# Performance work log

Hardware: AMD Instinct MI355X
Metric: run time of the kernel (lower is better)

## Reference

```python
import jax, jax.numpy as jnp
import numpy as np
from jax import lax

NUM_ENT = 100000
NUM_REL = 100          # init_rel has 2*NUM_REL rows (forward + inverse relations)
DIM = 200              # init_dim = gcn_dim = embed_dim
E = 1000000
B = 1024
K_H, K_W = 10, 20      # embed_dim == k_h * k_w
NUM_FILT = 200
KER = 7
FLAT_H = 2 * K_H - KER + 1   # 14
FLAT_W = K_W - KER + 1       # 14
FLAT_SZ = FLAT_H * FLAT_W * NUM_FILT  # 39200


def _bn1d(x, g, b, eps=1e-5):
    # training-mode BatchNorm1d (biased variance, matching torch)
    m = x.mean(0)
    v = x.var(0)
    return (x - m) * lax.rsqrt(v + eps) * g + b


def _bn2d(x, g, b, eps=1e-5):
    m = x.mean((0, 2, 3), keepdims=True)
    v = x.var((0, 2, 3), keepdims=True)
    return (x - m) * lax.rsqrt(v + eps) * g[None, :, None, None] + b[None, :, None, None]


def _compgcn_layer(x, r, src, dst, etype, enorm,
                   w_in, w_out, w_loop, w_rel, loop_rel, bias, gamma, beta):
    # CompGCNCov with opn='mult': comp(h_src, rel) = h_src * rel
    half = etype.shape[0] // 2
    comp = x[src] * r[etype]                                   # [E, din] edge gather + compose
    msg = jnp.concatenate([comp[:half] @ w_in,                 # first half: original edges
                           comp[half:] @ w_out], axis=0)       # second half: inverse edges
    msg = msg * enorm[:, None]
    agg = jax.ops.segment_sum(msg, dst, num_segments=NUM_ENT)  # scatter-sum to dst nodes
    loop = (x * loop_rel) @ w_loop                             # self-loop composition
    h = (agg + loop) * (1.0 / 3.0) + bias
    h = _bn1d(h, gamma, beta)
    return jnp.tanh(h), r @ w_rel


def setup_inputs() -> dict:
    key = jax.random.key(0)
    ks = jax.random.split(key, 40)
    f32 = jnp.float32
    s = 1.0 / np.sqrt(DIM)
    inp = {
        "init_embed": jax.random.normal(ks[0], (NUM_ENT, DIM), f32) * s,
        "init_rel":   jax.random.normal(ks[1], (2 * NUM_REL, DIM), f32) * s,
        "edge_norm":  jax.random.uniform(ks[2], (E,), f32),
    }
    names = ["w_in", "w_out", "w_loop", "w_rel"]
    for layer in (1, 2):
        for i, n in enumerate(names):
            inp[f"{n}{layer}"] = jax.random.normal(ks[3 + 6 * layer + i], (DIM, DIM), f32) * s
        inp[f"loop_rel{layer}"] = jax.random.normal(jax.random.fold_in(key, layer), (1, DIM), f32) * s
        inp[f"b{layer}"] = jnp.zeros((DIM,), f32)
        inp[f"g{layer}"] = jnp.ones((DIM,), f32)
        inp[f"be{layer}"] = jnp.zeros((DIM,), f32)
    inp["conv_w"] = jax.random.normal(ks[20], (NUM_FILT, 1, KER, KER), f32) * (1.0 / KER)
    inp["conv_b"] = jnp.zeros((NUM_FILT,), f32)
    inp["fc_w"] = jax.random.normal(ks[21], (DIM, FLAT_SZ), f32) * (1.0 / np.sqrt(FLAT_SZ))
    inp["fc_b"] = jnp.zeros((DIM,), f32)
    for n, c in (("bn0", 1), ("bn1", NUM_FILT), ("bn2", DIM)):
        inp[f"{n}_g"] = jnp.ones((c,), f32)
        inp[f"{n}_b"] = jnp.zeros((c,), f32)
    inp["subj"] = jax.random.randint(ks[22], (B,), 0, NUM_ENT)
    inp["rel_idx"] = jax.random.randint(ks[23], (B,), 0, 2 * NUM_REL)
    inp["obj"] = jax.random.randint(ks[24], (B,), 0, NUM_ENT)
    inp["src"] = jax.random.randint(ks[25], (E,), 0, NUM_ENT)
    inp["dst"] = jax.random.randint(ks[26], (E,), 0, NUM_ENT)
    inp["edge_type"] = jnp.concatenate([
        jax.random.randint(ks[27], (E // 2,), 0, NUM_REL),          # in-edges
        jax.random.randint(ks[28], (E // 2,), NUM_REL, 2 * NUM_REL)])  # inverse edges
    return inp


def reference(init_embed, init_rel, edge_norm,
              w_in1, w_out1, w_loop1, w_rel1, loop_rel1, b1, g1, be1,
              w_in2, w_out2, w_loop2, w_rel2, loop_rel2, b2, g2, be2,
              conv_w, conv_b, fc_w, fc_b,
              bn0_g, bn0_b, bn1_g, bn1_b, bn2_g, bn2_b,
              subj, rel_idx, obj, src, dst, edge_type):
    # --- GCN encoder: 2 CompGCN layers ---
    x, r = _compgcn_layer(init_embed, init_rel, src, dst, edge_type, edge_norm,
                          w_in1, w_out1, w_loop1, w_rel1, loop_rel1, b1, g1, be1)
    x, r = _compgcn_layer(x, r, src, dst, edge_type, edge_norm,
                          w_in2, w_out2, w_loop2, w_rel2, loop_rel2, b2, g2, be2)
    sub_emb, rel_emb, obj_emb = x[subj], r[rel_idx], x[obj]   # [B, DIM] each
    # --- ConvE scoring head ---
    stk = jnp.concatenate([sub_emb[:, None, :], rel_emb[:, None, :]], 1)
    stk = stk.reshape(B, 1, 2 * K_H, K_W)                     # [B,1,20,20]
    h = _bn2d(stk, bn0_g, bn0_b)
    h = lax.conv_general_dilated(h, conv_w, (1, 1), 'VALID',
                                 dimension_numbers=('NCHW', 'OIHW', 'NCHW'))
    h = h + conv_b[None, :, None, None]                       # [B,NUM_FILT,14,14]
    h = jnp.maximum(_bn2d(h, bn1_g, bn1_b), 0.0)
    h = h.reshape(B, FLAT_SZ) @ fc_w.T + fc_b                 # [B, DIM]
    h = jnp.maximum(_bn1d(h, bn2_g, bn2_b), 0.0)
    return jax.nn.sigmoid(h @ obj_emb.T)                      # [B, B]
```

## Files before the change

### kernel.cpp

```cpp
#include <hip/hip_runtime.h>

#define DIM 200
#define NENT 100000
#define NEDGE 1000000
#define EHALF 500000
#define NB 1024
#define NFILT 200
#define FLATSZ 39200

#define NDF ((size_t)NENT * DIM)
#define REGF ((size_t)20100000)

#define PANEL_TOT_H 6656
#define Y1OFF_H 3584
#define WT_TOTAL_H 139776

typedef float floatx4 __attribute__((ext_vector_type(4)));
typedef _Float16 halfx8 __attribute__((ext_vector_type(8)));
typedef _Float16 halfx4 __attribute__((ext_vector_type(4)));

__device__ __forceinline__ void gAtomicAdd(float* p, float v) { unsafeAtomicAdd(p, v); }
__device__ __forceinline__ void gAtomicAdd(double* p, double v) { unsafeAtomicAdd(p, v); }

__device__ __forceinline__ void gload16h(const _Float16* g, _Float16* l) {
    __builtin_amdgcn_global_load_lds(
        (const __attribute__((address_space(1))) void*)g,
        (__attribute__((address_space(3))) void*)l,
        16, 0, 0);
}

__global__ __launch_bounds__(256) void edge_hist(
    const int* __restrict__ dst, int* __restrict__ hist)
{
    int stride = gridDim.x * blockDim.x;
    for (int e = blockIdx.x * 256 + threadIdx.x; e < NEDGE; e += stride)
        atomicAdd(&hist[dst[e]], 1);
}

__global__ __launch_bounds__(256) void scan1(
    const int* __restrict__ hist, int* __restrict__ incl, int* __restrict__ bsum)
{
    __shared__ int sm[256];
    int i = blockIdx.x * 256 + threadIdx.x;
    int t = threadIdx.x;
    sm[t] = (i < NENT) ? hist[i] : 0;
    __syncthreads();
    for (int off = 1; off < 256; off <<= 1) {
        int v = (t >= off) ? sm[t - off] : 0;
        __syncthreads();
        sm[t] += v;
        __syncthreads();
    }
    if (i < NENT) incl[i] = sm[t];
    if (t == 255) bsum[blockIdx.x] = sm[255];
}

__global__ __launch_bounds__(512) void scan2(int* bsum, int nb)
{
    __shared__ int sm[512];
    int t = threadIdx.x;
    int v = (t < nb) ? bsum[t] : 0;
    sm[t] = v;
    __syncthreads();
    for (int off = 1; off < 512; off <<= 1) {
        int u = (t >= off) ? sm[t - off] : 0;
        __syncthreads();
        sm[t] += u;
        __syncthreads();
    }
    if (t < nb) bsum[t] = sm[t] - v;
}

__global__ __launch_bounds__(256) void scan3(
    const int* __restrict__ hist, int* __restrict__ offs,
    const int* __restrict__ bsum, int* __restrict__ cursor)
{
    int i = blockIdx.x * 256 + threadIdx.x;
    if (i < NENT) {
        int excl = offs[i] - hist[i] + bsum[blockIdx.x];
        offs[i] = excl;
        cursor[i] = excl;
    }
    if (i == 0) offs[NENT] = NEDGE;
}

__global__ __launch_bounds__(256) void edge_fill(
    const int* __restrict__ src, const int* __restrict__ dst,
    const int* __restrict__ etype, const float* __restrict__ enorm,
    int* __restrict__ cursor, int4* __restrict__ recs)
{
    int stride = gridDim.x * blockDim.x;
    for (int e = blockIdx.x * 256 + threadIdx.x; e < NEDGE; e += stride) {
        int pos = atomicAdd(&cursor[dst[e]], 1);
        recs[pos] = make_int4(src[e], etype[e] | ((e >= EHALF) ? 0x10000 : 0),
                              __float_as_int(enorm[e]), 0);
    }
}

__global__ __launch_bounds__(256) void build_map(
    const int* __restrict__ subj, const int* __restrict__ obj, int* __restrict__ map)
{
    int i = blockIdx.x * 256 + threadIdx.x;
    if (i < NB) map[subj[i]] = i;
    else if (i < 2 * NB) map[obj[i - NB]] = i;
}

__global__ __launch_bounds__(256) void to_f16(
    const float* __restrict__ X, _Float16* __restrict__ Y, long n4)
{
    long stride = (long)gridDim.x * blockDim.x;
    for (long i = (long)blockIdx.x * blockDim.x + threadIdx.x; i < n4; i += stride) {
        float4 v = ((const float4*)X)[i];
        halfx4 h;
        h[0] = (_Float16)v.x; h[1] = (_Float16)v.y;
        h[2] = (_Float16)v.z; h[3] = (_Float16)v.w;
        ((halfx4*)Y)[i] = h;
    }
}

__global__ __launch_bounds__(256) void gather_nodes(
    const _Float16* __restrict__ x16, const float* __restrict__ r,
    const int* __restrict__ offs, const int4* __restrict__ recs,
    _Float16* __restrict__ aggI, _Float16* __restrict__ aggO)
{
    int node = blockIdx.x * 4 + (threadIdx.x >> 6);
    int lane = threadIdx.x & 63;
    if (node >= NENT) return;
    int beg = offs[node], end = offs[node + 1];
    bool act = lane < 50;
    int lane_c = min(lane, 49);
    const float4* rb = (const float4*)r;
    float4 aI = make_float4(0.f, 0.f, 0.f, 0.f);
    float4 aO = make_float4(0.f, 0.f, 0.f, 0.f);

    auto ld_x = [&](int s) -> float4 {
        halfx4 v = *(const halfx4*)&x16[(size_t)s * 200 + lane_c * 4];
        return make_float4((float)v[0], (float)v[1], (float)v[2], (float)v[3]);
    };

    if (beg < end) {
        int i1 = min(beg + 1, end - 1);
        int4 rcA = recs[beg];
        int4 rcB = recs[i1];
        float4 xvA = ld_x(rcA.x);
        float4 rvA = rb[(size_t)(rcA.y & 0xffff) * 50 + lane_c];
        for (int i = beg; i < end; ++i) {
            int i2 = min(i + 2, end - 1);
            int4 rcC = recs[i2];
            float4 xvB = ld_x(rcB.x);
            float4 rvB = rb[(size_t)(rcB.y & 0xffff) * 50 + lane_c];
            float w = __int_as_float(rcA.z);
            float wI = (rcA.y & 0x10000) ? 0.f : w;
            float wO = w - wI;
            float px = xvA.x * rvA.x, py = xvA.y * rvA.y,
                  pz = xvA.z * rvA.z, pw = xvA.w * rvA.w;
            aI.x += px * wI; aI.y += py * wI; aI.z += pz * wI; aI.w += pw * wI;
            aO.x += px * wO; aO.y += py * wO; aO.z += pz * wO; aO.w += pw * wO;
            rcA = rcB; rcB = rcC; xvA = xvB; rvA = rvB;
        }
    }
    if (act) {
        halfx4 hI, hO;
        hI[0] = (_Float16)aI.x; hI[1] = (_Float16)aI.y;
        hI[2] = (_Float16)aI.z; hI[3] = (_Float16)aI.w;
        hO[0] = (_Float16)aO.x; hO[1] = (_Float16)aO.y;
        hO[2] = (_Float16)aO.z; hO[3] = (_Float16)aO.w;
        size_t base = (size_t)node * 200 + lane * 4;
        *(halfx4*)&aggI[base] = hI;
        *(halfx4*)&aggO[base] = hO;
    }
}

__global__ __launch_bounds__(256) void pack_w3(
    const float* __restrict__ w0, const float* __restrict__ w1,
    const float* __restrict__ w2, const float* __restrict__ lrel,
    _Float16* __restrict__ WpP)
{
    int i = blockIdx.x * 256 + threadIdx.x;
    if (i >= WT_TOTAL_H) return;
    int p = i / PANEL_TOT_H;
    int r = i % PANEL_TOT_H;
    int y = (r >= Y1OFF_H) ? 1 : 0;
    int rr = y ? (r - Y1OFF_H) : r;
    int rl = rr >> 5;
    int qx = (rr >> 3) & 3;
    int e = rr & 7;
    int q = qx ^ ((rl >> 1) & 3);
    int n = y * 112 + rl;
    int seg = p / 7, c = p - seg * 7;
    int k = c * 32 + q * 8 + e;
    const float* W = (seg == 0) ? w0 : (seg == 1) ? w1 : w2;
    float v = (n < 200 && k < 200) ? W[k * 200 + n] : 0.f;
    if (seg == 2 && n < 200 && k < 200) v *= lrel[k];
    WpP[i] = (_Float16)v;
}

__global__ __launch_bounds__(256) void pack_fcw(
    const float* __restrict__ W, _Float16* __restrict__ Wt)
{
    long i = (long)blockIdx.x * 256 + threadIdx.x;
    if (i >= (long)208 * FLATSZ) return;
    int n = (int)(i / FLATSZ);
    Wt[i] = (n < 200) ? (_Float16)W[i] : (_Float16)0.f;
}

template<int Y>
__global__ __launch_bounds__(1024) void gemm_big(
    const _Float16* __restrict__ A0h, const _Float16* __restrict__ A1h,
    const _Float16* __restrict__ A2h, const _Float16* __restrict__ WpP,
    float* __restrict__ C, const float* __restrict__ bias,
    const int* __restrict__ map, float alpha,
    double* __restrict__ s1, double* __restrict__ s2)
{
    constexpr int NF = Y ? 6 : 7;
    constexpr int PC = NF;
    constexpr int PANEL_H = NF * 512;
    constexpr int YOFF_H = Y ? Y1OFF_H : 0;
    constexpr int SEG_LDS_H = 7 * PANEL_H;
    __shared__ _Float16 Sb[2 * SEG_LDS_H];
    __shared__ float fsum[NF * 16];
    __shared__ float fsq[NF * 16];

    int tid = threadIdx.x;
    int lane = tid & 63, wave = tid >> 6;
    int col16 = lane & 15, quad = lane >> 4;
    if (tid < NF * 16) { fsum[tid] = 0.f; fsq[tid] = 0.f; }

    int gw = blockIdx.x * 16 + wave;
    bool act = gw < 3125;
    int t = act ? gw : 0;
    int r0 = t * 32 + col16, r1 = r0 + 16;
    size_t b0 = (size_t)r0 * 200, b1 = (size_t)r1 * 200;

    floatx4 acc[NF][2];
#pragma unroll
    for (int nf = 0; nf < NF; ++nf) { acc[nf][0] = (floatx4)0.f; acc[nf][1] = (floatx4)0.f; }

    halfx8 ca0, ca1, na0, na1;

    auto stage = [&](int seg, int bufi) {
        for (int cc = wave; cc < 7 * PC; cc += 16) {
            int p7 = cc / PC, sub = cc - p7 * PC;
            const _Float16* g = WpP + (size_t)(seg * 7 + p7) * PANEL_TOT_H
                              + YOFF_H + sub * 512 + lane * 8;
            gload16h(g, Sb + bufi * SEG_LDS_H + cc * 512);
        }
    };
    auto loadA = [&](int kc, halfx8& a0, halfx8& a1) {
        int seg = kc / 7, c = kc - seg * 7;
        int koff = c * 32 + quad * 8;
        if (koff < 200) {
            const _Float16* A = (seg == 0) ? A0h : (seg == 1) ? A1h : A2h;
            a0 = *(const halfx8*)&A[b0 + koff];
            a1 = *(const halfx8*)&A[b1 + koff];
        } else {
            a0 = (halfx8)0; a1 = (halfx8)0;
        }
    };

    stage(0, 0);
    if (act) loadA(0, ca0, ca1);
    __syncthreads();

    int buf = 0;
    for (int seg = 0; seg < 3; ++seg) {
        if (seg < 2) stage(seg + 1, buf ^ 1);
        if (act) {
#pragma unroll
            for (int c = 0; c < 7; ++c) {
                int kc = seg * 7 + c;
                if (kc < 20) loadA(kc + 1, na0, na1);
                const _Float16* P = Sb + buf * SEG_LDS_H + c * PANEL_H;
                __builtin_amdgcn_s_setprio(1);
#pragma unroll
                for (int nf = 0; nf < NF; ++nf) {
                    int rl = nf * 16 + col16;
                    int qs = quad ^ ((rl >> 1) & 3);
                    halfx8 b = *(const halfx8*)&P[rl * 32 + qs * 8];
                    acc[nf][0] = __builtin_amdgcn_mfma_f32_16x16x32_f16(ca0, b, acc[nf][0], 0, 0, 0);
                    acc[nf][1] = __builtin_amdgcn_mfma_f32_16x16x32_f16(ca1, b, acc[nf][1], 0, 0, 0);
                }
                __builtin_amdgcn_s_setprio(0);
                ca0 = na0; ca1 = na1;
            }
        }
        __syncthreads();
        buf ^= 1;
    }

    int slot[2][4];
    if (map && act) {
#pragma unroll
        for (int h = 0; h < 2; ++h)
#pragma unroll
            for (int j = 0; j < 4; ++j)
                slot[h][j] = map[t * 32 + h * 16 + quad * 4 + j];
    }
    if (act) {
#pragma unroll
        for (int nf = 0; nf < NF; ++nf) {
            int lc = nf * 16 + col16;
            int colg = Y * 112 + lc;
            float ls = 0.f, lq = 0.f;
            if (colg < 200) {
                float bv = bias[colg];
#pragma unroll
                for (int h = 0; h < 2; ++h) {
                    int rbase = t * 32 + h * 16 + quad * 4;
#pragma unroll
                    for (int j = 0; j < 4; ++j) {
                        float v = acc[nf][h][j] * alpha + bv;
                        ls += v; lq += v * v;
                        if (!map) {
                            C[(size_t)(rbase + j) * 200 + colg] = v;
                        } else {
                            int s = slot[h][j];
                            if (s >= 0) C[(size_t)s * 200 + colg] = v;
                        }
                    }
                }
            }
            ls += __shfl_down(ls, 32); ls += __shfl_down(ls, 16);
            lq += __shfl_down(lq, 32); lq += __shfl_down(lq, 16);
            if (quad == 0 && colg < 200) {
                atomicAdd(&fsum[lc], ls);
                atomicAdd(&fsq[lc], lq);
            }
        }
    }
    __syncthreads();
    if (tid < NF * 16) {
        int colg = Y * 112 + tid;
        if (colg < 200) {
            gAtomicAdd(&s1[colg], (double)fsum[tid]);
            gAtomicAdd(&s2[colg], (double)fsq[tid]);
        }
    }
}

template<int NF0, int NF>
__device__ __forceinline__ void fc_gemm_body(
    const _Float16* __restrict__ Ph, const _Float16* __restrict__ Wt,
    float* __restrict__ part, int ky, _Float16* Bs)
{
    int t = threadIdx.x;
    int lane = t & 63, wave = t >> 6;
    int col16 = lane & 15, quad = lane >> 4;
    int row_base = blockIdx.x * 128 + wave * 32;
    int c0 = ky * 25;
    floatx4 acc[NF][2];
#pragma unroll
    for (int nf = 0; nf < NF; ++nf) { acc[nf][0] = (floatx4)0.f; acc[nf][1] = (floatx4)0.f; }
    int r0 = row_base + col16, r1 = row_base + 16 + col16;
    const int rows4 = NF * 16 * 4;

    for (int c = c0; c < c0 + 25; ++c) {
        int k0 = c * 32;
        for (int i = t; i < rows4; i += 256) {
            int nl = i >> 2, part_i = i & 3;
            int n = NF0 * 16 + nl;
            *(halfx8*)&Bs[nl * 40 + part_i * 8] =
                *(const halfx8*)&Wt[(size_t)n * FLATSZ + k0 + part_i * 8];
        }
        __syncthreads();
        int koff = k0 + quad * 8;
        halfx8 a0 = *(const halfx8*)&Ph[(size_t)r0 * FLATSZ + koff];
        halfx8 a1 = *(const halfx8*)&Ph[(size_t)r1 * FLATSZ + koff];
#pragma unroll
        for (int nf = 0; nf < NF; ++nf) {
            halfx8 b = *(const halfx8*)&Bs[(nf * 16 + col16) * 40 + quad * 8];
            acc[nf][0] = __builtin_amdgcn_mfma_f32_16x16x32_f16(a0, b, acc[nf][0], 0, 0, 0);
            acc[nf][1] = __builtin_amdgcn_mfma_f32_16x16x32_f16(a1, b, acc[nf][1], 0, 0, 0);
        }
        __syncthreads();
    }
    float* out = part + (size_t)ky * (NB * 200);
#pragma unroll
    for (int nf = 0; nf < NF; ++nf) {
        int colg = NF0 * 16 + nf * 16 + col16;
        if (colg >= 200) continue;
#pragma unroll
        for (int h = 0; h < 2; ++h) {
            int rbase = row_base + h * 16 + quad * 4;
#pragma unroll
            for (int j = 0; j < 4; ++j)
                out[(size_t)(rbase + j) * 200 + colg] = acc[nf][h][j];
        }
    }
}

__global__ __launch_bounds__(256) void fc_gemm(
    const _Float16* __restrict__ Ph, const _Float16* __restrict__ Wt,
    float* __restrict__ part)
{
    __shared__ _Float16 Bs[112 * 40];
    int ky = blockIdx.y >> 1;
    if ((blockIdx.y & 1) == 0)
        fc_gemm_body<0, 7>(Ph, Wt, part, ky, Bs);
    else
        fc_gemm_body<7, 6>(Ph, Wt, part, ky, Bs);
}

__global__ __launch_bounds__(256) void fc_reduce(
    const float* __restrict__ part, const float* __restrict__ bias,
    float* __restrict__ hfc)
{
    int i = blockIdx.x * 256 + threadIdx.x;
    float acc = bias[i % 200];
#pragma unroll
    for (int y = 0; y < 49; ++y) acc += part[(size_t)y * (NB * 200) + i];
    hfc[i] = acc;
}

__global__ __launch_bounds__(256) void colstats(
    const float* __restrict__ X, int M, int rpb,
    double* __restrict__ s1, double* __restrict__ s2)
{
    int c = threadIdx.x;
    if (c >= 200) return;
    int r0 = blockIdx.x * rpb;
    int r1 = min(r0 + rpb, M);
    float sum = 0.f, sq = 0.f;
    for (int rr = r0; rr < r1; ++rr) {
        float v = X[(size_t)rr * 200 + c];
        sum += v; sq += v * v;
    }
    gAtomicAdd(&s1[c], (double)sum);
    gAtomicAdd(&s2[c], (double)sq);
}

__global__ void finalize_stats(const double* __restrict__ s1, const double* __restrict__ s2,
                               const float* __restrict__ g, const float* __restrict__ bb,
                               float* __restrict__ sc, float* __restrict__ sh,
                               int ncols, double count)
{
    int c = threadIdx.x;
    if (c >= ncols) return;
    double m = s1[c] / count;
    double v = s2[c] / count - m * m;
    double scd = (double)g[c] / sqrt(v + 1e-5);
    sc[c] = (float)scd;
    sh[c] = (float)((double)bb[c] - m * scd);
}

__global__ __launch_bounds__(256) void bn_tanh_f16(
    const float* __restrict__ X, const float* __restrict__ sc,
    const float* __restrict__ sh, _Float16* __restrict__ Y, long n4)
{
    long stride = (long)gridDim.x * blockDim.x;
    for (long i = (long)blockIdx.x * blockDim.x + threadIdx.x; i < n4; i += stride) {
        int c4 = (int)(i % 50) * 4;
        float4 v = ((const float4*)X)[i];
        halfx4 h;
        h[0] = (_Float16)tanhf(v.x * sc[c4 + 0] + sh[c4 + 0]);
        h[1] = (_Float16)tanhf(v.y * sc[c4 + 1] + sh[c4 + 1]);
        h[2] = (_Float16)tanhf(v.z * sc[c4 + 2] + sh[c4 + 2]);
        h[3] = (_Float16)tanhf(v.w * sc[c4 + 3] + sh[c4 + 3]);
        ((halfx4*)Y)[i] = h;
    }
}

__global__ __launch_bounds__(256) void bn_act_200(
    float* __restrict__ X, const float* __restrict__ sc, const float* __restrict__ sh,
    long n4, int act)
{
    long stride = (long)gridDim.x * blockDim.x;
    for (long i = (long)blockIdx.x * blockDim.x + threadIdx.x; i < n4; i += stride) {
        int c4 = (int)(i % 50) * 4;
        float4 v = ((const float4*)X)[i];
        float a0 = v.x * sc[c4 + 0] + sh[c4 + 0];
        float a1 = v.y * sc[c4 + 1] + sh[c4 + 1];
        float a2 = v.z * sc[c4 + 2] + sh[c4 + 2];
        float a3 = v.w * sc[c4 + 3] + sh[c4 + 3];
        if (act == 0) { a0 = tanhf(a0); a1 = tanhf(a1); a2 = tanhf(a2); a3 = tanhf(a3); }
        else { a0 = fmaxf(a0, 0.f); a1 = fmaxf(a1, 0.f); a2 = fmaxf(a2, 0.f); a3 = fmaxf(a3, 0.f); }
        ((float4*)X)[i] = make_float4(a0, a1, a2, a3);
    }
}

__global__ __launch_bounds__(256) void rel_mm(
    const float* __restrict__ R, const float* __restrict__ W, float* __restrict__ O)
{
    int idx = blockIdx.x * blockDim.x + threadIdx.x;
    if (idx >= 200 * 200) return;
    int row = idx / 200, col = idx - row * 200;
    float acc = 0.f;
    for (int k = 0; k < 200; ++k) acc = fmaf(R[row * 200 + k], W[k * 200 + col], acc);
    O[idx] = acc;
}

__global__ __launch_bounds__(256) void build_stk(
    const float* __restrict__ x2c, const float* __restrict__ r2,
    const int* __restrict__ subj, const int* __restrict__ ridx,
    const int* __restrict__ map,
    float* __restrict__ stk, double* __restrict__ s1, double* __restrict__ s2)
{
    __shared__ float wsum[4], wsq[4];
    int b = blockIdx.x, t = threadIdx.x;
    const float* se = x2c + (size_t)map[subj[b]] * DIM;
    const float* re = r2 + (size_t)ridx[b] * DIM;
    float sum = 0.f, sq = 0.f;
    for (int i = t; i < 400; i += 256) {
        float v = (i < 200) ? se[i] : re[i - 200];
        stk[(size_t)b * 400 + i] = v;
        sum += v; sq += v * v;
    }
    for (int off = 32; off > 0; off >>= 1) {
        sum += __shfl_down(sum, off);
        sq  += __shfl_down(sq, off);
    }
    if ((t & 63) == 0) { wsum[t >> 6] = sum; wsq[t >> 6] = sq; }
    __syncthreads();
    if (t == 0) {
        float S = wsum[0] + wsum[1] + wsum[2] + wsum[3];
        float Q = wsq[0] + wsq[1] + wsq[2] + wsq[3];
        gAtomicAdd(&s1[0], (double)S);
        gAtomicAdd(&s2[0], (double)Q);
    }
}

__global__ __launch_bounds__(256) void conv_fwd(
    const float* __restrict__ stk, const float* __restrict__ conv_w,
    const float* __restrict__ conv_b, const float* __restrict__ sc0,
    const float* __restrict__ sh0, _Float16* __restrict__ Ph,
    double* __restrict__ s1, double* __restrict__ s2)
{
    __shared__ float img[400];
    __shared__ float wsm[9800];
    __shared__ float bsm[200];
    __shared__ float fsum[200];
    __shared__ float fsq[200];
    int b = blockIdx.x, t = threadIdx.x;
    float scale0 = sc0[0], shift0 = sh0[0];
    if (t < 200) { fsum[t] = 0.f; fsq[t] = 0.f; bsm[t] = conv_b[t]; }
    for (int i = t; i < 400; i += 256) img[i] = stk[(size_t)b * 400 + i] * scale0 + shift0;
    for (int i = t; i < 9800; i += 256) wsm[i] = conv_w[i];
    __syncthreads();
    for (int fy = t; fy < 2800; fy += 256) {
        int f = fy / 14, y = fy - (fy / 14) * 14;
        const float* wf = &wsm[f * 49];
        float acc[14];
        float bias = bsm[f];
#pragma unroll
        for (int xx = 0; xx < 14; ++xx) acc[xx] = bias;
#pragma unroll
        for (int i = 0; i < 7; ++i) {
            const float* rowp = &img[(y + i) * 20];
            float rv[20];
#pragma unroll
            for (int c = 0; c < 20; ++c) rv[c] = rowp[c];
#pragma unroll
            for (int j = 0; j < 7; ++j) {
                float wv = wf[i * 7 + j];
#pragma unroll
                for (int xx = 0; xx < 14; ++xx) acc[xx] = fmaf(rv[xx + j], wv, acc[xx]);
            }
        }
        float ls = 0.f, lq = 0.f;
        _Float16* pp = Ph + (size_t)b * FLATSZ + (size_t)f * 196 + y * 14;
#pragma unroll
        for (int xx = 0; xx < 14; ++xx) {
            float v = acc[xx];
            pp[xx] = (_Float16)v;
            ls += v; lq += v * v;
        }
        atomicAdd(&fsum[f], ls);
        atomicAdd(&fsq[f], lq);
    }
    __syncthreads();
    if (t < 200) {
        gAtomicAdd(&s1[t], (double)fsum[t]);
        gAtomicAdd(&s2[t], (double)fsq[t]);
    }
}

__global__ __launch_bounds__(256) void bn1_relu_f16(
    _Float16* __restrict__ Ph, const float* __restrict__ sc, const float* __restrict__ sh)
{
    long n4 = (long)NB * (FLATSZ / 4);
    long stride = (long)gridDim.x * blockDim.x;
    for (long i = (long)blockIdx.x * blockDim.x + threadIdx.x; i < n4; i += stride) {
        int k4 = (int)(i % (FLATSZ / 4));
        int f = k4 / 49;
        float s = sc[f], h = sh[f];
        halfx4 v = ((const halfx4*)Ph)[i];
#pragma unroll
        for (int e = 0; e < 4; ++e) {
            float x = (float)v[e];
            x = fmaxf(x * s + h, 0.f);
            v[e] = (_Float16)x;
        }
        ((halfx4*)Ph)[i] = v;
    }
}

__global__ __launch_bounds__(256) void score_mm(
    const float* __restrict__ Hn, const float* __restrict__ x2c,
    const int* __restrict__ obj, const int* __restrict__ map,
    float* __restrict__ out)
{
    __shared__ float Asm[16][17];
    __shared__ float Bsm[16][17];
    int tx = threadIdx.x & 15, ty = threadIdx.x >> 4;
    int row = blockIdx.y * 16 + ty;
    int col = blockIdx.x * 16 + tx;
    int oj = map[obj[blockIdx.x * 16 + ty]];
    float acc = 0.f;
    for (int k0 = 0; k0 < 200; k0 += 16) {
        int k = k0 + tx;
        Asm[ty][tx] = (k < 200) ? Hn[(size_t)row * 200 + k] : 0.f;
        Bsm[ty][tx] = (k < 200) ? x2c[(size_t)oj * 200 + k] : 0.f;
        __syncthreads();
#pragma unroll
        for (int kk = 0; kk < 16; ++kk) acc = fmaf(Asm[ty][kk], Bsm[tx][kk], acc);
        __syncthreads();
    }
    out[(size_t)row * NB + col] = 1.f / (1.f + expf(-acc));
}

extern "C" void kernel_launch(void* const* d_in, const int* in_sizes, int n_in,
                              void* d_out, int out_size, void* d_ws, size_t ws_size,
                              hipStream_t stream)
{
    (void)in_sizes; (void)n_in; (void)out_size;
    const float* init_embed = (const float*)d_in[0];
    const float* init_rel   = (const float*)d_in[1];
    const float* edge_norm  = (const float*)d_in[2];
    const float* w_in1  = (const float*)d_in[3];
    const float* w_out1 = (const float*)d_in[4];
    const float* w_loop1= (const float*)d_in[5];
    const float* w_rel1 = (const float*)d_in[6];
    const float* lrel1  = (const float*)d_in[7];
    const float* b1     = (const float*)d_in[8];
    const float* gm1    = (const float*)d_in[9];
    const float* be1    = (const float*)d_in[10];
    const float* w_in2  = (const float*)d_in[11];
    const float* w_out2 = (const float*)d_in[12];
    const float* w_loop2= (const float*)d_in[13];
    const float* w_rel2 = (const float*)d_in[14];
    const float* lrel2  = (const float*)d_in[15];
    const float* b2     = (const float*)d_in[16];
    const float* gm2    = (const float*)d_in[17];
    const float* be2    = (const float*)d_in[18];
    const float* conv_w = (const float*)d_in[19];
    const float* conv_b = (const float*)d_in[20];
    const float* fc_w   = (const float*)d_in[21];
    const float* fc_b   = (const float*)d_in[22];
    const float* bn0_g  = (const float*)d_in[23];
    const float* bn0_b  = (const float*)d_in[24];
    const float* bn1_g  = (const float*)d_in[25];
    const float* bn1_b  = (const float*)d_in[26];
    const float* bn2_g  = (const float*)d_in[27];
    const float* bn2_b  = (const float*)d_in[28];
    const int* subj   = (const int*)d_in[29];
    const int* relidx = (const int*)d_in[30];
    const int* obj    = (const int*)d_in[31];
    const int* src    = (const int*)d_in[32];
    const int* dst    = (const int*)d_in[33];
    const int* etype  = (const int*)d_in[34];

    float* ws = (float*)d_ws;
    float* R0 = ws;
    float* R1 = ws + REGF;
    float* R2 = ws + 2 * REGF;
    float* p = ws + 3 * REGF;
    float* r1v = p;            p += 40000;
    float* r2v = p;            p += 40000;
    float* stk = p;            p += 409600;
    float* hfc = p;            p += 204800;
    float* x2c = p;            p += 409600;
    float* fsc = p;            p += 256;
    float* fsh = p;            p += 256;
    double* ds1 = (double*)p;  p += 512;
    double* ds2 = (double*)p;  p += 512;
    _Float16* Wp = (_Float16*)p; p += (WT_TOTAL_H + 1) / 2;
    int* map = (int*)p;        p += NENT;
    int* hist = (int*)p;       p += NENT;
    int* offs = (int*)p;       p += NENT + 4;
    int* cursor = (int*)p;     p += NENT;
    int* bsum = (int*)p;       p += 512;
    int4* recs = (int4*)p;     p += (size_t)NEDGE * 4;

    float* x1f = R0;
    _Float16* aggI1 = (_Float16*)R1;
    _Float16* ie16  = (_Float16*)(R1 + 10050000);
    _Float16* aggOh = (_Float16*)R2;
    _Float16* x1h = (_Float16*)R1;
    _Float16* aggI2 = (_Float16*)R0;
    _Float16* Ph  = (_Float16*)R0;
    _Float16* fch = (_Float16*)R2;
    float* fpart = R2 + 4200000;

    const size_t NEED = (size_t)(p - ws) * sizeof(float);
    if (ws_size < NEED) return;

    const int NBLK = (NENT + 255) / 256;
    const size_t DSBYTES = 512 * sizeof(double);

    hipMemsetAsync(hist, 0, NENT * sizeof(int), stream);
    hipMemsetAsync(map, 0xFF, NENT * sizeof(int), stream);
    edge_hist<<<1024, 256, 0, stream>>>(dst, hist);
    scan1<<<NBLK, 256, 0, stream>>>(hist, offs, bsum);
    scan2<<<1, 512, 0, stream>>>(bsum, NBLK);
    scan3<<<NBLK, 256, 0, stream>>>(hist, offs, bsum, cursor);
    edge_fill<<<1024, 256, 0, stream>>>(src, dst, etype, edge_norm, cursor, recs);
    build_map<<<(2 * NB + 255) / 256, 256, 0, stream>>>(subj, obj, map);

    const int PACK_BLKS = (WT_TOTAL_H + 255) / 256;

    pack_w3<<<PACK_BLKS, 256, 0, stream>>>(w_in1, w_out1, w_loop1, lrel1, Wp);
    to_f16<<<4096, 256, 0, stream>>>(init_embed, ie16, (long)NENT * 50);
    gather_nodes<<<(NENT + 3) / 4, 256, 0, stream>>>(ie16, init_rel, offs, recs,
                                                     aggI1, aggOh);
    hipMemsetAsync(ds1, 0, DSBYTES, stream);
    gemm_big<0><<<256, 1024, 0, stream>>>(aggI1, aggOh, ie16, Wp,
                                          x1f, b1, nullptr, 1.f / 3.f, ds1, ds2);
    gemm_big<1><<<256, 1024, 0, stream>>>(aggI1, aggOh, ie16, Wp,
                                          x1f, b1, nullptr, 1.f / 3.f, ds1, ds2);
    finalize_stats<<<1, 256, 0, stream>>>(ds1, ds2, gm1, be1, fsc, fsh, 200, (double)NENT);
    bn_tanh_f16<<<4096, 256, 0, stream>>>(x1f, fsc, fsh, x1h, (long)NENT * 50);
    rel_mm<<<(40000 + 255) / 256, 256, 0, stream>>>(init_rel, w_rel1, r1v);

    pack_w3<<<PACK_BLKS, 256, 0, stream>>>(w_in2, w_out2, w_loop2, lrel2, Wp);
    gather_nodes<<<(NENT + 3) / 4, 256, 0, stream>>>(x1h, r1v, offs, recs,
                                                     aggI2, aggOh);
    hipMemsetAsync(ds1, 0, DSBYTES, stream);
    gemm_big<0><<<256, 1024, 0, stream>>>(aggI2, aggOh, x1h, Wp,
                                          x2c, b2, map, 1.f / 3.f, ds1, ds2);
    gemm_big<1><<<256, 1024, 0, stream>>>(aggI2, aggOh, x1h, Wp,
                                          x2c, b2, map, 1.f / 3.f, ds1, ds2);
    finalize_stats<<<1, 256, 0, stream>>>(ds1, ds2, gm2, be2, fsc, fsh, 200, (double)NENT);
    bn_act_200<<<400, 256, 0, stream>>>(x2c, fsc, fsh, (long)2 * NB * 50, 0);
    rel_mm<<<(40000 + 255) / 256, 256, 0, stream>>>(r1v, w_rel2, r2v);

    hipMemsetAsync(ds1, 0, DSBYTES, stream);
    build_stk<<<NB, 256, 0, stream>>>(x2c, r2v, subj, relidx, map, stk, ds1, ds2);
    finalize_stats<<<1, 256, 0, stream>>>(ds1, ds2, bn0_g, bn0_b, fsc, fsh, 1,
                                          (double)((long)NB * 400));
    hipMemsetAsync(ds1, 0, DSBYTES, stream);
    conv_fwd<<<NB, 256, 0, stream>>>(stk, conv_w, conv_b, fsc, fsh, Ph, ds1, ds2);
    finalize_stats<<<1, 256, 0, stream>>>(ds1, ds2, bn1_g, bn1_b, fsc, fsh, 200,
                                          (double)((long)NB * 196));
    bn1_relu_f16<<<4096, 256, 0, stream>>>(Ph, fsc, fsh);
    pack_fcw<<<(int)(((long)208 * FLATSZ + 255) / 256), 256, 0, stream>>>(fc_w, fch);
    fc_gemm<<<dim3(8, 98), 256, 0, stream>>>(Ph, fch, fpart);
    fc_reduce<<<800, 256, 0, stream>>>(fpart, fc_b, hfc);
    hipMemsetAsync(ds1, 0, DSBYTES, stream);
    colstats<<<4, 256, 0, stream>>>(hfc, NB, 256, ds1, ds2);
    finalize_stats<<<1, 256, 0, stream>>>(ds1, ds2, bn2_g, bn2_b, fsc, fsh, 200, (double)NB);
    bn_act_200<<<200, 256, 0, stream>>>(hfc, fsc, fsh, (long)NB * 50, 1);
    score_mm<<<dim3(NB / 16, NB / 16), 256, 0, stream>>>(hfc, x2c, obj, map, (float*)d_out);
}
```

Baseline: 1.071 ms.

## Use fp16 relation table and packed fp16 accumulation in edge gather

Converts the relation embeddings to fp16 before each gather pass and performs the edge compose-and-accumulate in packed halfx4 arithmetic instead of fp32. The gather prefetch depth is also increased from two to three edges ahead. The aim is to cut the gather's memory traffic and ALU work, but accumulating a node's sum over many edges in fp16 loses precision and can overflow for high-degree nodes. It also adds a small conversion launch per layer.

```diff
diff --git a/kernel.cpp b/kernel.cpp
--- a/kernel.cpp
+++ b/kernel.cpp
@@ -119,7 +119,7 @@
 }
 
 __global__ __launch_bounds__(256) void gather_nodes(
-    const _Float16* __restrict__ x16, const float* __restrict__ r,
+    const _Float16* __restrict__ x16, const _Float16* __restrict__ r16,
     const int* __restrict__ offs, const int4* __restrict__ recs,
     _Float16* __restrict__ aggI, _Float16* __restrict__ aggO)
 {
@@ -129,45 +129,46 @@
     int beg = offs[node], end = offs[node + 1];
     bool act = lane < 50;
     int lane_c = min(lane, 49);
-    const float4* rb = (const float4*)r;
-    float4 aI = make_float4(0.f, 0.f, 0.f, 0.f);
-    float4 aO = make_float4(0.f, 0.f, 0.f, 0.f);
-
-    auto ld_x = [&](int s) -> float4 {
-        halfx4 v = *(const halfx4*)&x16[(size_t)s * 200 + lane_c * 4];
-        return make_float4((float)v[0], (float)v[1], (float)v[2], (float)v[3]);
+    halfx4 aI = (halfx4)0, aO = (halfx4)0;
+
+    auto ld_x = [&](int s) -> halfx4 {
+        return *(const halfx4*)&x16[(size_t)s * 200 + lane_c * 4];
+    };
+    auto ld_r = [&](int et) -> halfx4 {
+        return *(const halfx4*)&r16[(size_t)et * 200 + lane_c * 4];
     };
 
     if (beg < end) {
         int i1 = min(beg + 1, end - 1);
+        int i2 = min(beg + 2, end - 1);
         int4 rcA = recs[beg];
         int4 rcB = recs[i1];
-        float4 xvA = ld_x(rcA.x);
-        float4 rvA = rb[(size_t)(rcA.y & 0xffff) * 50 + lane_c];
+        int4 rcC = recs[i2];
+        halfx4 xvA = ld_x(rcA.x), xvB = ld_x(rcB.x);
+        halfx4 rvA = ld_r(rcA.y & 0xffff), rvB = ld_r(rcB.y & 0xffff);
         for (int i = beg; i < end; ++i) {
-            int i2 = min(i + 2, end - 1);
-            int4 rcC = recs[i2];
-            float4 xvB = ld_x(rcB.x);
-            float4 rvB = rb[(size_t)(rcB.y & 0xffff) * 50 + lane_c];
+            int i3 = min(i + 3, end - 1);
+            int4 rcD = recs[i3];
+            halfx4 xvC = ld_x(rcC.x);
+            halfx4 rvC = ld_r(rcC.y & 0xffff);
             float w = __int_as_float(rcA.z);
             float wI = (rcA.y & 0x10000) ? 0.f : w;
             float wO = w - wI;
-            float px = xvA.x * rvA.x, py = xvA.y * rvA.y,
-                  pz = xvA.z * rvA.z, pw = xvA.w * rvA.w;
-            aI.x += px * wI; aI.y += py * wI; aI.z += pz * wI; aI.w += pw * wI;
-            aO.x += px * wO; aO.y += py * wO; aO.z += pz * wO; aO.w += pw * wO;
-            rcA = rcB; rcB = rcC; xvA = xvB; rvA = rvB;
+            _Float16 wIh = (_Float16)wI, wOh = (_Float16)wO;
+            halfx4 wI4 = {wIh, wIh, wIh, wIh};
+            halfx4 wO4 = {wOh, wOh, wOh, wOh};
+            halfx4 comp = xvA * rvA;
+            aI += comp * wI4;
+            aO += comp * wO4;
+            rcA = rcB; rcB = rcC; rcC = rcD;
+            xvA = xvB; xvB = xvC;
+            rvA = rvB; rvB = rvC;
         }
     }
     if (act) {
-        halfx4 hI, hO;
-        hI[0] = (_Float16)aI.x; hI[1] = (_Float16)aI.y;
-        hI[2] = (_Float16)aI.z; hI[3] = (_Float16)aI.w;
-        hO[0] = (_Float16)aO.x; hO[1] = (_Float16)aO.y;
-        hO[2] = (_Float16)aO.z; hO[3] = (_Float16)aO.w;
         size_t base = (size_t)node * 200 + lane * 4;
-        *(halfx4*)&aggI[base] = hI;
-        *(halfx4*)&aggO[base] = hO;
+        *(halfx4*)&aggI[base] = aI;
+        *(halfx4*)&aggO[base] = aO;
     }
 }
 
@@ -674,6 +675,7 @@
     double* ds1 = (double*)p;  p += 512;
     double* ds2 = (double*)p;  p += 512;
     _Float16* Wp = (_Float16*)p; p += (WT_TOTAL_H + 1) / 2;
+    _Float16* rg16 = (_Float16*)p; p += 20000;
     int* map = (int*)p;        p += NENT;
     int* hist = (int*)p;       p += NENT;
     int* offs = (int*)p;       p += NENT + 4;
@@ -710,7 +712,8 @@
 
     pack_w3<<<PACK_BLKS, 256, 0, stream>>>(w_in1, w_out1, w_loop1, lrel1, Wp);
     to_f16<<<4096, 256, 0, stream>>>(init_embed, ie16, (long)NENT * 50);
-    gather_nodes<<<(NENT + 3) / 4, 256, 0, stream>>>(ie16, init_rel, offs, recs,
+    to_f16<<<40, 256, 0, stream>>>(init_rel, rg16, 10000);
+    gather_nodes<<<(NENT + 3) / 4, 256, 0, stream>>>(ie16, rg16, offs, recs,
                                                      aggI1, aggOh);
     hipMemsetAsync(ds1, 0, DSBYTES, stream);
     gemm_big<0><<<256, 1024, 0, stream>>>(aggI1, aggOh, ie16, Wp,
@@ -722,7 +725,8 @@
     rel_mm<<<(40000 + 255) / 256, 256, 0, stream>>>(init_rel, w_rel1, r1v);
 
     pack_w3<<<PACK_BLKS, 256, 0, stream>>>(w_in2, w_out2, w_loop2, lrel2, Wp);
-    gather_nodes<<<(NENT + 3) / 4, 256, 0, stream>>>(x1h, r1v, offs, recs,
+    to_f16<<<40, 256, 0, stream>>>(r1v, rg16, 10000);
+    gather_nodes<<<(NENT + 3) / 4, 256, 0, stream>>>(x1h, rg16, offs, recs,
                                                      aggI2, aggOh);
     hipMemsetAsync(ds1, 0, DSBYTES, stream);
     gemm_big<0><<<256, 1024, 0, stream>>>(aggI2, aggOh, x1h, Wp,
```

Result: no change. 1.066 ms (-0.5%).
